# Kernel optimization log

Measured on AMD Instinct MI355X. Metric: run time of the kernel, lower is better.

The kernel has to match this reference:

```python
import jax, jax.numpy as jnp
import numpy as np

NUM_USERS = 100000
NUM_ITEMS = 50000
EMBED_DIM = 128
NNZ = 2000000
N_LAYERS = 3


def setup_inputs() -> dict:
    key = jax.random.key(0)
    k1, k2, k3, k4, k5 = jax.random.split(key, 5)
    stdv = 1.0 / np.sqrt(EMBED_DIM)
    user_pref = jax.random.uniform(k1, (NUM_USERS, EMBED_DIM), jnp.float32, -stdv, stdv)
    item_pref = jax.random.uniform(k2, (NUM_ITEMS, EMBED_DIM), jnp.float32, -stdv, stdv)
    vals = jax.random.uniform(k3, (NNZ,), jnp.float32)
    rows = jax.random.randint(k4, (NNZ,), 0, NUM_USERS, jnp.int32)
    cols = jax.random.randint(k5, (NNZ,), 0, NUM_ITEMS, jnp.int32)
    return {"user_pref": user_pref, "item_pref": item_pref, "vals": vals,
            "rows": rows, "cols": cols}


def _spmm(vals, src_idx, dst_idx, x, num_out):
    # y[dst] += vals * x[src]  — SpMM over COO edge list
    msgs = vals[:, None] * x[src_idx]            # [nnz, D]
    return jax.ops.segment_sum(msgs, dst_idx, num_segments=num_out)


def reference(user_pref, item_pref, vals, rows, cols):
    u, it = user_pref, item_pref
    u_sum, i_sum = user_pref, item_pref
    for _ in range(N_LAYERS):
        # u_next = Graph @ item_layer ; i_next = Graph.T @ user_layer (same layer index)
        u_next = _spmm(vals, cols, rows, it, NUM_USERS)   # [U, D]
        i_next = _spmm(vals, rows, cols, u, NUM_ITEMS)    # [I, D]
        u, it = u_next, i_next
        u_sum = u_sum + u
        i_sum = i_sum + it
    inv = 1.0 / (N_LAYERS + 1)
    return (u_sum * inv, i_sum * inv)
```

## Files before the change

kernel.cpp:

```cpp
#include <hip/hip_runtime.h>


#define NUM_USERS 100000
#define NUM_ITEMS 50000
#define EMBED_DIM 128
#define NNZ_COUNT 2000000
#define NBUCK_U 391
#define NBUCK_I 196
#define EPB 8192
#define NBLK 245


__device__ __forceinline__ unsigned bf16_rnd(float f) {
    unsigned u = __float_as_uint(f);
    return (u + 0x7FFFu + ((u >> 16) & 1u)) >> 16;
}
__device__ __forceinline__ unsigned pack_bf16(float x, float y) {
    return bf16_rnd(x) | (bf16_rnd(y) << 16);
}

__global__ __launch_bounds__(256) void to_bf16_dual(
    const float* __restrict__ a, unsigned* __restrict__ oa, int na8,
    const float* __restrict__ b, unsigned* __restrict__ ob, int nb8)
{
    int i = blockIdx.x * 256 + threadIdx.x;
    const float4* s4; uint4* d4;
    if (i < na8) {
        s4 = reinterpret_cast<const float4*>(a) + i * 2;
        d4 = reinterpret_cast<uint4*>(oa) + i;
    } else {
        i -= na8;
        if (i >= nb8) return;
        s4 = reinterpret_cast<const float4*>(b) + i * 2;
        d4 = reinterpret_cast<uint4*>(ob) + i;
    }
    float4 x = s4[0], y = s4[1];
    uint4 r;
    r.x = pack_bf16(x.x, x.y); r.y = pack_bf16(x.z, x.w);
    r.z = pack_bf16(y.x, y.y); r.w = pack_bf16(y.z, y.w);
    *d4 = r;
}


__global__ __launch_bounds__(256) void msplit_hist(
    const int* __restrict__ rows, const int* __restrict__ cols,
    int* __restrict__ hist_u, int* __restrict__ hist_i)
{
    __shared__ int h[NBUCK_U + NBUCK_I];
    for (int i = threadIdx.x; i < NBUCK_U + NBUCK_I; i += 256) h[i] = 0;
    __syncthreads();
    const int base = blockIdx.x * EPB;
    const int end = min(base + EPB, NNZ_COUNT);
    for (int e = base + threadIdx.x; e < end; e += 256) {
        atomicAdd(&h[rows[e] >> 8], 1);
        atomicAdd(&h[NBUCK_U + (cols[e] >> 8)], 1);
    }
    __syncthreads();
    for (int b = threadIdx.x; b < NBUCK_U; b += 256)
        hist_u[b * NBLK + blockIdx.x] = h[b];
    for (int b = threadIdx.x; b < NBUCK_I; b += 256)
        hist_i[b * NBLK + blockIdx.x] = h[NBUCK_U + b];
}

__global__ __launch_bounds__(256) void msplit_offsets(
    const int* __restrict__ hist_u, const int* __restrict__ hist_i,
    int* __restrict__ offs_u, int* __restrict__ offs_i,
    int* __restrict__ tot_u, int* __restrict__ tot_i)
{
    __shared__ int buf[256];
    int b = blockIdx.x;
    const int* hist; int* offs; int* tot; int nbuck;
    if (b < NBUCK_U) { hist = hist_u; offs = offs_u; tot = tot_u; nbuck = NBUCK_U; }
    else { b -= NBUCK_U; hist = hist_i; offs = offs_i; tot = tot_i; nbuck = NBUCK_I; }
    const int t = threadIdx.x;
    const int x = (t < NBLK) ? hist[b * NBLK + t] : 0;
    buf[t] = x;
    __syncthreads();
    for (int d = 1; d < 256; d <<= 1) {
        const int y = (t >= d) ? buf[t - d] : 0;
        __syncthreads();
        buf[t] += y;
        __syncthreads();
    }
    if (t < NBLK) offs[t * nbuck + b] = buf[t] - x;
    if (t == 255) tot[b] = buf[255];
}

__global__ __launch_bounds__(512) void scan_buckets(
    const int* __restrict__ tot_u, int* __restrict__ bbase_u,
    const int* __restrict__ tot_i, int* __restrict__ bbase_i)
{
    __shared__ int buf[512];
    const int t = threadIdx.x;
    const int* tot; int* bbase; int nb;
    if (blockIdx.x == 0) { tot = tot_u; bbase = bbase_u; nb = NBUCK_U; }
    else                 { tot = tot_i; bbase = bbase_i; nb = NBUCK_I; }
    const int v = (t < nb) ? tot[t] : 0;
    buf[t] = v;
    __syncthreads();
    for (int d = 1; d < 512; d <<= 1) {
        const int y = (t >= d) ? buf[t - d] : 0;
        __syncthreads();
        buf[t] += y;
        __syncthreads();
    }
    if (t <= nb) bbase[t] = buf[t] - v;
}

__global__ __launch_bounds__(256) void msplit_scatter(
    const int* __restrict__ rows, const int* __restrict__ cols,
    const float* __restrict__ vals,
    const int* __restrict__ offs_u, const int* __restrict__ offs_i,
    const int* __restrict__ bbase_u, const int* __restrict__ bbase_i,
    int2* __restrict__ stage_u, int2* __restrict__ stage_i)
{
    __shared__ int cu[NBUCK_U];
    __shared__ int ci[NBUCK_I];
    const int t = threadIdx.x;
    for (int b = t; b < NBUCK_U; b += 256)
        cu[b] = offs_u[blockIdx.x * NBUCK_U + b] + bbase_u[b];
    for (int b = t; b < NBUCK_I; b += 256)
        ci[b] = offs_i[blockIdx.x * NBUCK_I + b] + bbase_i[b];
    __syncthreads();
    const int base = blockIdx.x * EPB;
    const int end = min(base + EPB, NNZ_COUNT);
    for (int e = base + t; e < end; e += 256) {
        const int r = rows[e];
        const int c = cols[e];
        const int vb = __float_as_int(vals[e]);
        const int su = atomicAdd(&cu[r >> 8], 1);
        stage_u[su] = make_int2(c | ((r & 255) << 16), vb);
        const int si = atomicAdd(&ci[c >> 8], 1);
        stage_i[si] = make_int2(r | ((c & 255) << 17), vb);
    }
}

__global__ __launch_bounds__(256) void bucket_build(
    const int* __restrict__ bbase_u, const int2* __restrict__ stage_u,
    unsigned* __restrict__ pairs_u, int* __restrict__ ptr_u,
    const int* __restrict__ bbase_i, const int2* __restrict__ stage_i,
    unsigned* __restrict__ pairs_i, int* __restrict__ ptr_i)
{
    __shared__ int hcnt[256];
    __shared__ int buf[256];
    __shared__ int cur[256];
    const int t = threadIdx.x;
    int b = blockIdx.x;
    const bool uside = (b < NBUCK_U);
    const int* bbase; const int2* stage; unsigned* pairs; int* ptr; int n; int sh;
    if (uside) { bbase = bbase_u; stage = stage_u; pairs = pairs_u; ptr = ptr_u; n = NUM_USERS; sh = 16; }
    else { b -= NBUCK_U; bbase = bbase_i; stage = stage_i; pairs = pairs_i; ptr = ptr_i; n = NUM_ITEMS; sh = 17; }
    const int beg = bbase[b];
    const int end = bbase[b + 1];

    hcnt[t] = 0;
    __syncthreads();
    for (int idx = beg + t; idx < end; idx += 256)
        atomicAdd(&hcnt[(stage[idx].x >> sh) & 255], 1);
    __syncthreads();

    const int v = hcnt[t];
    buf[t] = v;
    __syncthreads();
    for (int d = 1; d < 256; d <<= 1) {
        const int y = (t >= d) ? buf[t - d] : 0;
        __syncthreads();
        buf[t] += y;
        __syncthreads();
    }
    const int rowbase = beg + buf[t] - v;
    cur[t] = rowbase;
    const int first = b << 8;
    if (first + t < n) ptr[first + t] = rowbase;
    if (first + t == n) ptr[n] = end;
    else if (first + 256 == n && t == 0) ptr[n] = end;
    __syncthreads();

    for (int idx = beg + t; idx < end; idx += 256) {
        const int2 s = stage[idx];
        const int local = (s.x >> sh) & 255;
        const unsigned vb = bf16_rnd(__int_as_float(s.y));
        unsigned packed;
        if (uside) packed = (unsigned)(s.x & 0xFFFF) | (vb << 16);
        else       packed = (unsigned)(s.x & 0x1FFFF) | ((vb & 0x7FFFu) << 17);
        const int slot = atomicAdd(&cur[local], 1);
        pairs[slot] = packed;
    }
}


template<bool USIDE>
__device__ __forceinline__ void decode_pair(unsigned s, int& c, float& v) {
    if (USIDE) { c = (int)(s & 0xFFFFu);  v = __uint_as_float(s & 0xFFFF0000u); }
    else       { c = (int)(s & 0x1FFFFu); v = __uint_as_float((s & 0xFFFE0000u) >> 1); }
}

template<int MODE, bool USIDE>
__device__ __forceinline__ void spmm_row_bf(
    const int* __restrict__ ptr, const unsigned* __restrict__ pairs,
    const unsigned* __restrict__ src, unsigned* __restrict__ dst,
    const unsigned* __restrict__ l1, const unsigned* __restrict__ l2,
    const float* __restrict__ base, float* __restrict__ out,
    int row, int lane)
{
    const int start = ptr[row];
    const int end   = ptr[row + 1];
    float2 acc = make_float2(0.f, 0.f);

    for (int chunk = start; chunk < end; chunk += 64) {
        const int idx = chunk + lane;
        const unsigned p = (idx < end) ? pairs[idx] : 0u;
        int m = end - chunk; if (m > 64) m = 64;

        int j = 0;
        for (; j + 8 <= m; j += 8) {
            unsigned sv[8]; int c[8]; float v[8]; unsigned g[8];
            #pragma unroll
            for (int k = 0; k < 8; ++k) sv[k] = (unsigned)__shfl((int)p, j + k);
            #pragma unroll
            for (int k = 0; k < 8; ++k) {
                decode_pair<USIDE>(sv[k], c[k], v[k]);
                g[k] = src[(size_t)c[k] * 64 + lane];
            }
            #pragma unroll
            for (int k = 0; k < 8; ++k) {
                acc.x += v[k] * __uint_as_float(g[k] << 16);
                acc.y += v[k] * __uint_as_float(g[k] & 0xFFFF0000u);
            }
        }
        for (; j < m; ++j) {
            const unsigned s = (unsigned)__shfl((int)p, j);
            int c; float v;
            decode_pair<USIDE>(s, c, v);
            const unsigned g = src[(size_t)c * 64 + lane];
            acc.x += v * __uint_as_float(g << 16);
            acc.y += v * __uint_as_float(g & 0xFFFF0000u);
        }
    }

    if (MODE == 0) {
        dst[(size_t)row * 64 + lane] = pack_bf16(acc.x, acc.y);
    } else {
        const unsigned a1 = l1[(size_t)row * 64 + lane];
        const unsigned a2 = l2[(size_t)row * 64 + lane];
        const size_t o = (size_t)row * EMBED_DIM + (lane << 1);
        const float2 bs = *reinterpret_cast<const float2*>(base + o);
        float2 r;
        r.x = (bs.x + __uint_as_float(a1 << 16) + __uint_as_float(a2 << 16) + acc.x) * 0.25f;
        r.y = (bs.y + __uint_as_float(a1 & 0xFFFF0000u) + __uint_as_float(a2 & 0xFFFF0000u) + acc.y) * 0.25f;
        *reinterpret_cast<float2*>(out + o) = r;
    }
}

template<int MODE>
__global__ __launch_bounds__(256) void csr_spmm_dual_bf(
    const int* __restrict__ ptr_u, const unsigned* __restrict__ pairs_u,
    const unsigned* __restrict__ src_u, unsigned* __restrict__ dst_u,
    const unsigned* __restrict__ l1_u, const unsigned* __restrict__ l2_u,
    const float* __restrict__ base_u, float* __restrict__ out_u,
    const int* __restrict__ ptr_i, const unsigned* __restrict__ pairs_i,
    const unsigned* __restrict__ src_i, unsigned* __restrict__ dst_i,
    const unsigned* __restrict__ l1_i, const unsigned* __restrict__ l2_i,
    const float* __restrict__ base_i, float* __restrict__ out_i,
    int GU)
{
    const int lane = threadIdx.x & 63;
    const int w = threadIdx.x >> 6;
    if ((int)blockIdx.x < GU) {
        const int row = blockIdx.x * 4 + w;
        if (row < NUM_USERS)
            spmm_row_bf<MODE, true>(ptr_u, pairs_u, src_u, dst_u, l1_u, l2_u, base_u, out_u, row, lane);
    } else {
        const int row = ((int)blockIdx.x - GU) * 4 + w;
        if (row < NUM_ITEMS)
            spmm_row_bf<MODE, false>(ptr_i, pairs_i, src_i, dst_i, l1_i, l2_i, base_i, out_i, row, lane);
    }
}


__global__ __launch_bounds__(256) void edge_spmm(
    const float* __restrict__ vals, const int* __restrict__ rows,
    const int* __restrict__ cols, const float* __restrict__ u_src,
    const float* __restrict__ i_src, float* __restrict__ u_dst,
    float* __restrict__ i_dst, int nnz)
{
    const int lane = threadIdx.x & 31;
    const int e = blockIdx.x * 8 + (threadIdx.x >> 5);
    if (e >= nnz) return;
    const float v = vals[e];
    const size_t ro = (size_t)rows[e] * EMBED_DIM + lane * 4;
    const size_t co = (size_t)cols[e] * EMBED_DIM + lane * 4;
    const float4 iv = *reinterpret_cast<const float4*>(i_src + co);
    const float4 uv = *reinterpret_cast<const float4*>(u_src + ro);
    atomicAdd(u_dst + ro + 0, v * iv.x); atomicAdd(u_dst + ro + 1, v * iv.y);
    atomicAdd(u_dst + ro + 2, v * iv.z); atomicAdd(u_dst + ro + 3, v * iv.w);
    atomicAdd(i_dst + co + 0, v * uv.x); atomicAdd(i_dst + co + 1, v * uv.y);
    atomicAdd(i_dst + co + 2, v * uv.z); atomicAdd(i_dst + co + 3, v * uv.w);
}

__global__ __launch_bounds__(256) void acc_scale(
    float* __restrict__ out, const float* __restrict__ x, long n, float scale)
{
    long i = ((long)blockIdx.x * blockDim.x + threadIdx.x) * 4;
    if (i >= n) return;
    float4 o = *reinterpret_cast<float4*>(out + i);
    float4 a = *reinterpret_cast<const float4*>(x + i);
    o.x = (o.x + a.x) * scale; o.y = (o.y + a.y) * scale;
    o.z = (o.z + a.z) * scale; o.w = (o.w + a.w) * scale;
    *reinterpret_cast<float4*>(out + i) = o;
}


extern "C" void kernel_launch(void* const* d_in, const int* in_sizes, int n_in,
                              void* d_out, int out_size, void* d_ws, size_t ws_size,
                              hipStream_t stream)
{
    const float* user = (const float*)d_in[0];
    const float* item = (const float*)d_in[1];
    const float* vals = (const float*)d_in[2];
    const int*   rows = (const int*)d_in[3];
    const int*   cols = (const int*)d_in[4];

    const size_t UD = (size_t)NUM_USERS * EMBED_DIM;
    const size_t ID = (size_t)NUM_ITEMS * EMBED_DIM;

    float* out_u = (float*)d_out;
    float* out_i = out_u + UD;

    char* ws = (char*)d_ws;
    unsigned* user_bf = (unsigned*)ws;              ws += UD * 2;
    unsigned* item_bf = (unsigned*)ws;              ws += ID * 2;
    unsigned* uA = (unsigned*)ws;                   ws += UD * 2;
    unsigned* uB = (unsigned*)ws;                   ws += UD * 2;
    unsigned* iA = (unsigned*)ws;                   ws += ID * 2;
    unsigned* iB = (unsigned*)ws;                   ws += ID * 2;
    unsigned* pairs_u = (unsigned*)ws;              ws += (size_t)NNZ_COUNT * 4;
    unsigned* pairs_i = (unsigned*)ws;              ws += (size_t)NNZ_COUNT * 4;
    int2* stage_u = (int2*)ws;                      ws += (size_t)NNZ_COUNT * 8;
    int2* stage_i = (int2*)ws;                      ws += (size_t)NNZ_COUNT * 8;
    int* ptr_u = (int*)ws;                          ws += (NUM_USERS + 1) * 4;
    int* ptr_i = (int*)ws;                          ws += (NUM_ITEMS + 1) * 4;
    int* bbase_u = (int*)ws;                        ws += (NBUCK_U + 1) * 4;
    int* bbase_i = (int*)ws;                        ws += (NBUCK_I + 1) * 4;
    const size_t REQ = (size_t)(ws - (char*)d_ws);

    int* hist_u = (int*)pairs_u;
    int* hist_i = hist_u + NBUCK_U * NBLK;
    int* offs_u = hist_i + NBUCK_I * NBLK;
    int* offs_i = offs_u + NBLK * NBUCK_U;
    int* tot_u  = offs_i + NBLK * NBUCK_I;
    int* tot_i  = tot_u + NBUCK_U;

    if (ws_size >= REQ) {
        const int NA8 = (int)(UD / 8), NB8 = (int)(ID / 8);
        to_bf16_dual<<<(NA8 + NB8 + 255) / 256, 256, 0, stream>>>(
            user, user_bf, NA8, item, item_bf, NB8);

        msplit_hist<<<NBLK, 256, 0, stream>>>(rows, cols, hist_u, hist_i);
        msplit_offsets<<<NBUCK_U + NBUCK_I, 256, 0, stream>>>(
            hist_u, hist_i, offs_u, offs_i, tot_u, tot_i);
        scan_buckets<<<2, 512, 0, stream>>>(tot_u, bbase_u, tot_i, bbase_i);
        msplit_scatter<<<NBLK, 256, 0, stream>>>(
            rows, cols, vals, offs_u, offs_i, bbase_u, bbase_i, stage_u, stage_i);
        bucket_build<<<NBUCK_U + NBUCK_I, 256, 0, stream>>>(
            bbase_u, stage_u, pairs_u, ptr_u,
            bbase_i, stage_i, pairs_i, ptr_i);

        const int GU = (NUM_USERS + 3) / 4;
        const int GI = (NUM_ITEMS + 3) / 4;

        csr_spmm_dual_bf<0><<<GU + GI, 256, 0, stream>>>(
            ptr_u, pairs_u, item_bf, uA, nullptr, nullptr, nullptr, nullptr,
            ptr_i, pairs_i, user_bf, iA, nullptr, nullptr, nullptr, nullptr, GU);
        csr_spmm_dual_bf<0><<<GU + GI, 256, 0, stream>>>(
            ptr_u, pairs_u, iA, uB, nullptr, nullptr, nullptr, nullptr,
            ptr_i, pairs_i, uA, iB, nullptr, nullptr, nullptr, nullptr, GU);
        csr_spmm_dual_bf<1><<<GU + GI, 256, 0, stream>>>(
            ptr_u, pairs_u, iB, nullptr, uA, uB, user, out_u,
            ptr_i, pairs_i, uB, nullptr, iA, iB, item, out_i, GU);
    } else {
        char* fw = (char*)d_ws;
        float* fuA = (float*)fw;                    fw += UD * 4;
        float* fuB = (float*)fw;                    fw += UD * 4;
        float* fiA = (float*)fw;                    fw += ID * 4;
        float* fiB = (float*)fw;                    fw += ID * 4;

        const int EDGE_BLOCKS = (NNZ_COUNT + 7) / 8;
        const int ACC_U = (int)(UD / 1024), ACC_I = (int)(ID / 1024);

        hipMemcpyAsync(out_u, user, UD * 4, hipMemcpyDeviceToDevice, stream);
        hipMemcpyAsync(out_i, item, ID * 4, hipMemcpyDeviceToDevice, stream);

        hipMemsetAsync(fuA, 0, UD * 4, stream);
        hipMemsetAsync(fiA, 0, ID * 4, stream);
        edge_spmm<<<EDGE_BLOCKS, 256, 0, stream>>>(vals, rows, cols, user, item, fuA, fiA, NNZ_COUNT);
        acc_scale<<<ACC_U, 256, 0, stream>>>(out_u, fuA, (long)UD, 1.0f);
        acc_scale<<<ACC_I, 256, 0, stream>>>(out_i, fiA, (long)ID, 1.0f);

        hipMemsetAsync(fuB, 0, UD * 4, stream);
        hipMemsetAsync(fiB, 0, ID * 4, stream);
        edge_spmm<<<EDGE_BLOCKS, 256, 0, stream>>>(vals, rows, cols, fuA, fiA, fuB, fiB, NNZ_COUNT);
        acc_scale<<<ACC_U, 256, 0, stream>>>(out_u, fuB, (long)UD, 1.0f);
        acc_scale<<<ACC_I, 256, 0, stream>>>(out_i, fiB, (long)ID, 1.0f);

        hipMemsetAsync(fuA, 0, UD * 4, stream);
        hipMemsetAsync(fiA, 0, ID * 4, stream);
        edge_spmm<<<EDGE_BLOCKS, 256, 0, stream>>>(vals, rows, cols, fuB, fiB, fuA, fiA, NNZ_COUNT);
        acc_scale<<<ACC_U, 256, 0, stream>>>(out_u, fuA, (long)UD, 0.25f);
        acc_scale<<<ACC_I, 256, 0, stream>>>(out_i, fiA, (long)ID, 0.25f);
    }
}
```

Baseline: 657.7 us.

## Add second radix pass so CSR neighbours are ordered by source bucket

Measured after the change: 708.2 us. 7.7% more time.

```diff
diff --git a/kernel.cpp b/kernel.cpp
--- a/kernel.cpp
+++ b/kernel.cpp
@@ -127,18 +127,87 @@
     for (int e = base + t; e < end; e += 256) {
         const int r = rows[e];
         const int c = cols[e];
-        const int vb = __float_as_int(vals[e]);
+        const unsigned vb = bf16_rnd(vals[e]);
         const int su = atomicAdd(&cu[r >> 8], 1);
-        stage_u[su] = make_int2(c | ((r & 255) << 16), vb);
+        stage_u[su] = make_int2((int)((unsigned)r | ((vb & 0x7FFFu) << 17)), c);
         const int si = atomicAdd(&ci[c >> 8], 1);
-        stage_i[si] = make_int2(r | ((c & 255) << 17), vb);
-    }
-}
-
-__global__ __launch_bounds__(256) void bucket_build(
-    const int* __restrict__ bbase_u, const int2* __restrict__ stage_u,
+        stage_i[si] = make_int2((int)((unsigned)c | (vb << 16)), r);
+    }
+}
+
+
+__global__ __launch_bounds__(256) void hist2_dual(
+    const int2* __restrict__ stage_i, const int2* __restrict__ stage_u,
+    int* __restrict__ h2_u, int* __restrict__ h2_i)
+{
+    __shared__ int h[NBUCK_U];
+    const bool uchain = (blockIdx.x < NBLK);
+    const int blk = uchain ? blockIdx.x : blockIdx.x - NBLK;
+    const int2* stage = uchain ? stage_i : stage_u;
+    int* h2 = uchain ? h2_u : h2_i;
+    const int nbuck = uchain ? NBUCK_U : NBUCK_I;
+    for (int i = threadIdx.x; i < nbuck; i += 256) h[i] = 0;
+    __syncthreads();
+    const int base = blk * EPB;
+    const int end = min(base + EPB, NNZ_COUNT);
+    for (int e = base + threadIdx.x; e < end; e += 256)
+        atomicAdd(&h[stage[e].y >> 8], 1);
+    __syncthreads();
+    for (int b = threadIdx.x; b < nbuck; b += 256)
+        h2[b * NBLK + blk] = h[b];
+}
+
+__global__ __launch_bounds__(256) void offsets2_dual(
+    const int* __restrict__ h2_u, const int* __restrict__ h2_i,
+    const int* __restrict__ bbase_u, const int* __restrict__ bbase_i,
+    int* __restrict__ o2_u, int* __restrict__ o2_i)
+{
+    __shared__ int buf[256];
+    int b = blockIdx.x;
+    const int* h2; const int* bbase; int* o2; int nbuck;
+    if (b < NBUCK_U) { h2 = h2_u; bbase = bbase_u; o2 = o2_u; nbuck = NBUCK_U; }
+    else { b -= NBUCK_U; h2 = h2_i; bbase = bbase_i; o2 = o2_i; nbuck = NBUCK_I; }
+    const int t = threadIdx.x;
+    const int x = (t < NBLK) ? h2[b * NBLK + t] : 0;
+    buf[t] = x;
+    __syncthreads();
+    for (int d = 1; d < 256; d <<= 1) {
+        const int y = (t >= d) ? buf[t - d] : 0;
+        __syncthreads();
+        buf[t] += y;
+        __syncthreads();
+    }
+    if (t < NBLK) o2[t * nbuck + b] = bbase[b] + buf[t] - x;
+}
+
+__global__ __launch_bounds__(256) void scatter2_dual(
+    const int2* __restrict__ stage_i, const int2* __restrict__ stage_u,
+    const int* __restrict__ o2_u, const int* __restrict__ o2_i,
+    int2* __restrict__ stage2_u, int2* __restrict__ stage2_i)
+{
+    __shared__ int cur[NBUCK_U];
+    const bool uchain = (blockIdx.x < NBLK);
+    const int blk = uchain ? blockIdx.x : blockIdx.x - NBLK;
+    const int2* stage = uchain ? stage_i : stage_u;
+    const int* o2 = uchain ? o2_u : o2_i;
+    int2* stage2 = uchain ? stage2_u : stage2_i;
+    const int nbuck = uchain ? NBUCK_U : NBUCK_I;
+    const int t = threadIdx.x;
+    for (int b = t; b < nbuck; b += 256) cur[b] = o2[blk * nbuck + b];
+    __syncthreads();
+    const int base = blk * EPB;
+    const int end = min(base + EPB, NNZ_COUNT);
+    for (int e = base + t; e < end; e += 256) {
+        const int2 s = stage[e];
+        const int slot = atomicAdd(&cur[s.y >> 8], 1);
+        stage2[slot] = s;
+    }
+}
+
+__global__ __launch_bounds__(256) void build_dual(
+    const int* __restrict__ bbase_u, const int2* __restrict__ stage2_u,
     unsigned* __restrict__ pairs_u, int* __restrict__ ptr_u,
-    const int* __restrict__ bbase_i, const int2* __restrict__ stage_i,
+    const int* __restrict__ bbase_i, const int2* __restrict__ stage2_i,
     unsigned* __restrict__ pairs_i, int* __restrict__ ptr_i)
 {
     __shared__ int hcnt[256];
@@ -147,16 +216,16 @@
     const int t = threadIdx.x;
     int b = blockIdx.x;
     const bool uside = (b < NBUCK_U);
-    const int* bbase; const int2* stage; unsigned* pairs; int* ptr; int n; int sh;
-    if (uside) { bbase = bbase_u; stage = stage_u; pairs = pairs_u; ptr = ptr_u; n = NUM_USERS; sh = 16; }
-    else { b -= NBUCK_U; bbase = bbase_i; stage = stage_i; pairs = pairs_i; ptr = ptr_i; n = NUM_ITEMS; sh = 17; }
+    const int* bbase; const int2* stage2; unsigned* pairs; int* ptr; int n;
+    if (uside) { bbase = bbase_u; stage2 = stage2_u; pairs = pairs_u; ptr = ptr_u; n = NUM_USERS; }
+    else { b -= NBUCK_U; bbase = bbase_i; stage2 = stage2_i; pairs = pairs_i; ptr = ptr_i; n = NUM_ITEMS; }
     const int beg = bbase[b];
     const int end = bbase[b + 1];
 
     hcnt[t] = 0;
     __syncthreads();
     for (int idx = beg + t; idx < end; idx += 256)
-        atomicAdd(&hcnt[(stage[idx].x >> sh) & 255], 1);
+        atomicAdd(&hcnt[stage2[idx].y & 255], 1);
     __syncthreads();
 
     const int v = hcnt[t];
@@ -177,14 +246,9 @@
     __syncthreads();
 
     for (int idx = beg + t; idx < end; idx += 256) {
-        const int2 s = stage[idx];
-        const int local = (s.x >> sh) & 255;
-        const unsigned vb = bf16_rnd(__int_as_float(s.y));
-        unsigned packed;
-        if (uside) packed = (unsigned)(s.x & 0xFFFF) | (vb << 16);
-        else       packed = (unsigned)(s.x & 0x1FFFF) | ((vb & 0x7FFFu) << 17);
-        const int slot = atomicAdd(&cur[local], 1);
-        pairs[slot] = packed;
+        const int2 s = stage2[idx];
+        const int slot = atomicAdd(&cur[s.y & 255], 1);
+        pairs[slot] = (unsigned)s.x;
     }
 }
 
@@ -351,6 +415,14 @@
     int* tot_u  = offs_i + NBLK * NBUCK_I;
     int* tot_i  = tot_u + NBUCK_U;
 
+    char* mid = (char*)uA;
+    int2* stage2_u = (int2*)mid;
+    int2* stage2_i = (int2*)(mid + (size_t)NNZ_COUNT * 8);
+    int* h2_u = (int*)(mid + (size_t)NNZ_COUNT * 16);
+    int* h2_i = h2_u + NBUCK_U * NBLK;
+    int* o2_u = h2_i + NBUCK_I * NBLK;
+    int* o2_i = o2_u + NBLK * NBUCK_U;
+
     if (ws_size >= REQ) {
         const int NA8 = (int)(UD / 8), NB8 = (int)(ID / 8);
         to_bf16_dual<<<(NA8 + NB8 + 255) / 256, 256, 0, stream>>>(
@@ -362,9 +434,15 @@
         scan_buckets<<<2, 512, 0, stream>>>(tot_u, bbase_u, tot_i, bbase_i);
         msplit_scatter<<<NBLK, 256, 0, stream>>>(
             rows, cols, vals, offs_u, offs_i, bbase_u, bbase_i, stage_u, stage_i);
-        bucket_build<<<NBUCK_U + NBUCK_I, 256, 0, stream>>>(
-            bbase_u, stage_u, pairs_u, ptr_u,
-            bbase_i, stage_i, pairs_i, ptr_i);
+
+        hist2_dual<<<2 * NBLK, 256, 0, stream>>>(stage_i, stage_u, h2_u, h2_i);
+        offsets2_dual<<<NBUCK_U + NBUCK_I, 256, 0, stream>>>(
+            h2_u, h2_i, bbase_u, bbase_i, o2_u, o2_i);
+        scatter2_dual<<<2 * NBLK, 256, 0, stream>>>(
+            stage_i, stage_u, o2_u, o2_i, stage2_u, stage2_i);
+        build_dual<<<NBUCK_U + NBUCK_I, 256, 0, stream>>>(
+            bbase_u, stage2_u, pairs_u, ptr_u,
+            bbase_i, stage2_i, pairs_i, ptr_i);
 
         const int GU = (NUM_USERS + 3) / 4;
         const int GI = (NUM_ITEMS + 3) / 4;
```
